# Performance work log

Hardware: AMD Instinct MI355X
Metric: run time of the kernel (lower is better)

## Reference

```python
import jax, jax.numpy as jnp
import numpy as np

D_MODEL = 1024
NUM_HEADS = 16
THETA = 10000.0
B, T = 2, 2048


def _rope(x, pos, theta_base):
    # x: (b, h, t, d_h); interleaved pairs (x0,x1),(x2,x3),... per the
    # rearrange '... (c d) -> ... c d' with d=2 in the original module.
    d = x.shape[-1]
    half = d // 2
    inv_freq = 1.0 / (theta_base ** (2.0 * jnp.arange(half, dtype=jnp.float32) / d))
    ang = pos.astype(jnp.float32)[:, None] * inv_freq[None, :]  # (t, half)
    sin = jnp.sin(ang)[None, None]  # (1,1,t,half)
    cos = jnp.cos(ang)[None, None]
    x1 = x[..., 0::2]
    x2 = x[..., 1::2]
    r1 = x1 * cos - x2 * sin
    r2 = x1 * sin + x2 * cos
    return jnp.stack([r1, r2], axis=-1).reshape(x.shape)


def setup_inputs() -> dict:
    key = jax.random.key(0)
    k0, k1, k2, k3, k4 = jax.random.split(key, 5)
    sigma = (2.0 / (D_MODEL + D_MODEL)) ** 0.5
    return {
        "in_features": jax.random.normal(k0, (B, T, D_MODEL), dtype=jnp.float32),
        "Wq": jax.random.normal(k1, (D_MODEL, D_MODEL), dtype=jnp.float32) * sigma,
        "Wk": jax.random.normal(k2, (D_MODEL, D_MODEL), dtype=jnp.float32) * sigma,
        "Wv": jax.random.normal(k3, (D_MODEL, D_MODEL), dtype=jnp.float32) * sigma,
        "Wo": jax.random.normal(k4, (D_MODEL, D_MODEL), dtype=jnp.float32) * sigma,
        "token_positions": jnp.arange(T, dtype=jnp.int32),
    }


def reference(in_features, Wq, Wk, Wv, Wo, token_positions):
    b, t, d_model = in_features.shape
    h = NUM_HEADS
    d_h = d_model // h
    # Fused-style QKV projections (x @ W.T, weights stored (in, out))
    q = in_features @ Wq.T
    k = in_features @ Wk.T
    v = in_features @ Wv.T
    # (b, t, h*d_h) -> (b, h, t, d_h)
    q = q.reshape(b, t, h, d_h).transpose(0, 2, 1, 3)
    k = k.reshape(b, t, h, d_h).transpose(0, 2, 1, 3)
    v = v.reshape(b, t, h, d_h).transpose(0, 2, 1, 3)
    q = _rope(q, token_positions, THETA)
    k = _rope(k, token_positions, THETA)
    scale = 1.0 / jnp.sqrt(jnp.asarray(d_h, dtype=q.dtype))
    scores = jnp.einsum('bhqd,bhkd->bhqk', q, k) * scale
    causal = jnp.tril(jnp.ones((t, t), dtype=bool))
    scores = jnp.where(causal[None, None], scores, -jnp.inf)
    attn = jax.nn.softmax(scores, axis=-1)
    out = jnp.einsum('bhqk,bhkd->bhqd', attn, v)
    out = out.transpose(0, 2, 1, 3).reshape(b, t, h * d_h)
    return out @ Wo.T
```

## Files before the change

### kernel.cpp

```cpp
#include <hip/hip_runtime.h>

#define D_MODEL 1024
#define NUM_HEADS 16
#define DH 64
#define B_SZ 2
#define T_SZ 2048
#define M_ROWS (B_SZ * T_SZ)

typedef __bf16 bf16;
typedef __bf16 bf16x4 __attribute__((ext_vector_type(4)));
typedef __bf16 bf16x8 __attribute__((ext_vector_type(8)));
typedef float f32x4 __attribute__((ext_vector_type(4)));

__device__ __forceinline__ void async_copy16(const bf16* g, bf16* l) {
  __builtin_amdgcn_global_load_lds(
      (const __attribute__((address_space(1))) void*)g,
      (__attribute__((address_space(3))) void*)l, 16, 0, 0);
}

#define NX (M_ROWS * D_MODEL / 4)
#define NW (D_MODEL * D_MODEL / 4)

__global__ __launch_bounds__(256) void cast_all(
    const float* __restrict__ X, const float* __restrict__ Wq,
    const float* __restrict__ Wk, const float* __restrict__ Wv,
    const float* __restrict__ Wo,
    bf16* __restrict__ Xb, bf16* __restrict__ Wqb, bf16* __restrict__ Wkb,
    bf16* __restrict__ Wvb, bf16* __restrict__ Wob) {
  int i = blockIdx.x * 256 + threadIdx.x;
  const float* s; bf16* d; int off;
  if (i < NX) {
    s = X; d = Xb; off = i;
  } else {
    int j = i - NX;
    int w = j >> 18;
    off = j & (NW - 1);
    if (w == 0)      { s = Wq; d = Wqb; }
    else if (w == 1) { s = Wk; d = Wkb; }
    else if (w == 2) { s = Wv; d = Wvb; }
    else             { s = Wo; d = Wob; }
  }
  float4 v = ((const float4*)s)[off];
  bf16x4 o;
  o[0] = (bf16)v.x; o[1] = (bf16)v.y; o[2] = (bf16)v.z; o[3] = (bf16)v.w;
  ((bf16x4*)d)[off] = o;
}

#define KLN 0.28782313662425f
#define BK 32
#define NKT (D_MODEL / BK)

__global__ __launch_bounds__(512, 4) void qkv_gemm(
    const bf16* __restrict__ Xb,
    const bf16* __restrict__ Wqb, const bf16* __restrict__ Wkb,
    const bf16* __restrict__ Wvb, const int* __restrict__ pos,
    bf16* __restrict__ Q, bf16* __restrict__ K, bf16* __restrict__ VT) {
  __shared__ bf16 LA[3][128 * BK];
  __shared__ bf16 LB[3][256 * BK];

  int tid = threadIdx.x;
  int wave = tid >> 6, lane = tid & 63;
  int wm = wave >> 2, wn = wave & 3;
  int l15 = lane & 15, quad = lane >> 4;

  int row0 = blockIdx.x * 128;
  int col0 = blockIdx.y * 256;
  int sel = col0 >> 10;
  int nb = col0 & 1023;
  const bf16* W = (sel == 0) ? Wqb : (sel == 1) ? Wkb : Wvb;

  int srow = tid >> 2;
  int scol = 8 * ((tid & 3) ^ ((tid >> 3) & 3));
  const bf16* Ag = Xb + (size_t)(row0 + srow) * D_MODEL + scol;
  const bf16* Bg = W + (size_t)(nb + srow) * D_MODEL + scol;
  int ldst = tid * 8;

  int swz = 8 * (quad ^ ((l15 >> 1) & 3));
  int aoff = (wm * 64 + l15) * BK + swz;
  int boff = (wn * 64 + l15) * BK + swz;

  f32x4 acc[4][4];
#pragma unroll
  for (int mi = 0; mi < 4; ++mi)
#pragma unroll
    for (int nj = 0; nj < 4; ++nj) acc[mi][nj] = (f32x4){0.f, 0.f, 0.f, 0.f};

#define STAGE(bq, pt)                                                        \
  do {                                                                       \
    int k0_ = (pt) * BK;                                                     \
    async_copy16(Ag + k0_, &LA[bq][ldst]);                                   \
    async_copy16(Bg + k0_, &LB[bq][ldst]);                                   \
    async_copy16(Bg + k0_ + (size_t)128 * D_MODEL, &LB[bq][ldst + 4096]);    \
  } while (0)

  STAGE(0, 0);
  STAGE(1, 1);
  asm volatile("s_waitcnt vmcnt(3)" ::: "memory");
  __builtin_amdgcn_s_barrier();
  __builtin_amdgcn_sched_barrier(0);

  int cur = 0;
  for (int kt = 0; kt < NKT; ++kt) {
    const bf16* La = LA[cur];
    const bf16* Lb = LB[cur];
    bf16x8 a[4], b[4];
#pragma unroll
    for (int mi = 0; mi < 4; ++mi)
      a[mi] = *(const bf16x8*)&La[aoff + mi * 16 * BK];
#pragma unroll
    for (int nj = 0; nj < 4; ++nj)
      b[nj] = *(const bf16x8*)&Lb[boff + nj * 16 * BK];

    if (kt + 2 < NKT) {
      int nbuf = cur + 2 >= 3 ? cur - 1 : cur + 2;
      STAGE(nbuf, kt + 2);
      asm volatile("s_waitcnt vmcnt(3) lgkmcnt(0)" ::: "memory");
    } else {
      asm volatile("s_waitcnt vmcnt(0) lgkmcnt(0)" ::: "memory");
    }
    __builtin_amdgcn_s_barrier();
    __builtin_amdgcn_sched_barrier(0);

    __builtin_amdgcn_s_setprio(1);
#pragma unroll
    for (int mi = 0; mi < 4; ++mi)
#pragma unroll
      for (int nj = 0; nj < 4; ++nj)
        acc[mi][nj] = __builtin_amdgcn_mfma_f32_16x16x32_bf16(
            a[mi], b[nj], acc[mi][nj], 0, 0, 0);
    __builtin_amdgcn_s_setprio(0);

    cur = cur == 2 ? 0 : cur + 1;
  }
#undef STAGE

  if (sel == 1) {
    bool even = (l15 & 1) == 0;
#pragma unroll
    for (int nj = 0; nj < 4; ++nj) {
      float fr = __expf(-(float)((nj * 16 + (l15 & 14)) >> 1) * KLN);
#pragma unroll
      for (int mi = 0; mi < 4; ++mi)
#pragma unroll
        for (int r = 0; r < 4; ++r) {
          float p = (float)pos[(row0 + wm * 64 + mi * 16 + quad * 4 + r) &
                               (T_SZ - 1)];
          float v = acc[mi][nj][r];
          float pn = __shfl_xor(v, 1);
          float s, c;
          __sincosf(p * fr, &s, &c);
          acc[mi][nj][r] = even ? (v * c - pn * s) : (pn * s + v * c);
        }
    }
  }

  if (sel == 2) {
    int b = row0 >> 11;
    int t0 = row0 & (T_SZ - 1);
#pragma unroll
    for (int mi = 0; mi < 4; ++mi) {
      int t = t0 + wm * 64 + mi * 16 + quad * 4;
#pragma unroll
      for (int nj = 0; nj < 4; ++nj) {
        int col = nb + wn * 64 + nj * 16 + l15;
        int h = col >> 6;
        int d = col & 63;
        bf16x4 ov;
#pragma unroll
        for (int r = 0; r < 4; ++r) ov[r] = (bf16)acc[mi][nj][r];
        *(bf16x4*)&VT[((size_t)(b * NUM_HEADS + h) * DH + d) * T_SZ + t] = ov;
      }
    }
  } else {
    bf16* Out = (sel == 0) ? Q : K;
#pragma unroll
    for (int mi = 0; mi < 4; ++mi) {
      int row = row0 + wm * 64 + mi * 16 + quad * 4;
#pragma unroll
      for (int nj = 0; nj < 4; ++nj) {
        int col = nb + wn * 64 + nj * 16 + l15;
#pragma unroll
        for (int r = 0; r < 4; ++r)
          Out[(size_t)(row + r) * D_MODEL + col] = (bf16)acc[mi][nj][r];
      }
    }
  }
}

#define PST 72
#define KST 72

__global__ __launch_bounds__(256) void attn_kernel(
    const bf16* __restrict__ Q, const bf16* __restrict__ K,
    const bf16* __restrict__ VT, const int* __restrict__ pos,
    bf16* __restrict__ AO) {
  __shared__ bf16 Kt[64 * KST];
  __shared__ bf16 Vt[64 * KST];
  __shared__ bf16 Pbuf[4][16 * PST];

  int bh = blockIdx.x;
  int y = blockIdx.y;
  int yq = y >> 3, yr = y & 7;
  int qi = 8 * yq + ((yq & 1) ? 7 - yr : yr);
  int bb = bh >> 4, h = bh & 15;
  int tid = threadIdx.x;
  int wave = tid >> 6, lane = tid & 63;
  int l15 = lane & 15, quad = lane >> 4;

  int q0 = qi * 64 + wave * 16;
  size_t grow = (size_t)bb * T_SZ + q0;

  const bf16* Qp = Q + (grow + l15) * D_MODEL + h * DH + quad * 8;
  bf16x8 bq0 = *(const bf16x8*)(Qp);
  bf16x8 bq1 = *(const bf16x8*)(Qp + 32);
  {
    float p = (float)pos[q0 + l15];
#pragma unroll
    for (int jj = 0; jj < 4; ++jj) {
      int i0 = quad * 4 + jj;
      float s, c;
      __sincosf(p * __expf(-(float)i0 * KLN), &s, &c);
      float x1 = (float)bq0[2 * jj], x2 = (float)bq0[2 * jj + 1];
      bq0[2 * jj]     = (bf16)(x1 * c - x2 * s);
      bq0[2 * jj + 1] = (bf16)(x1 * s + x2 * c);
      __sincosf(p * __expf(-(float)(i0 + 16) * KLN), &s, &c);
      float y1 = (float)bq1[2 * jj], y2 = (float)bq1[2 * jj + 1];
      bq1[2 * jj]     = (bf16)(y1 * c - y2 * s);
      bq1[2 * jj + 1] = (bf16)(y1 * s + y2 * c);
    }
  }

  f32x4 o[4];
#pragma unroll
  for (int nt = 0; nt < 4; ++nt) o[nt] = (f32x4){0.f, 0.f, 0.f, 0.f};
  float l_i = 0.f;

  int srow = tid >> 2;
  int sc = (tid & 3) * 16;
  const bf16* Kg = K + ((size_t)bb * T_SZ + srow) * D_MODEL + h * DH + sc;
  const bf16* Vg = VT + ((size_t)bh * DH + srow) * T_SZ + sc;
  bf16* Kl = &Kt[srow * KST + sc];
  bf16* Vl = &Vt[srow * KST + sc];

  bf16* Pw = Pbuf[wave];
  int nchunks = qi + 1;
  int rel = wave * 16 + l15;

  bf16x8 kr0 = *(const bf16x8*)(Kg);
  bf16x8 kr1 = *(const bf16x8*)(Kg + 8);
  bf16x8 vr0 = *(const bf16x8*)(Vg);
  bf16x8 vr1 = *(const bf16x8*)(Vg + 8);

  for (int t = 0; t < nchunks; ++t) {
    __syncthreads();
    *(bf16x8*)(Kl) = kr0;
    *(bf16x8*)(Kl + 8) = kr1;
    *(bf16x8*)(Vl) = vr0;
    *(bf16x8*)(Vl + 8) = vr1;
    if (t + 1 < nchunks) {
      const bf16* Kn = Kg + (size_t)(t + 1) * 64 * D_MODEL;
      const bf16* Vn = Vg + (t + 1) * 64;
      kr0 = *(const bf16x8*)(Kn);
      kr1 = *(const bf16x8*)(Kn + 8);
      vr0 = *(const bf16x8*)(Vn);
      vr1 = *(const bf16x8*)(Vn + 8);
    }
    __syncthreads();

    f32x4 st[4];
#pragma unroll
    for (int cs = 0; cs < 4; ++cs) {
      bf16x8 ak0 = *(const bf16x8*)&Kt[(cs * 16 + l15) * KST + quad * 8];
      bf16x8 ak1 = *(const bf16x8*)&Kt[(cs * 16 + l15) * KST + 32 + quad * 8];
      f32x4 s4 = (f32x4){0.f, 0.f, 0.f, 0.f};
      s4 = __builtin_amdgcn_mfma_f32_16x16x32_bf16(ak0, bq0, s4, 0, 0, 0);
      s4 = __builtin_amdgcn_mfma_f32_16x16x32_bf16(ak1, bq1, s4, 0, 0, 0);
      st[cs] = s4;
    }

    bool last = (t == nchunks - 1);
    float ps = 0.f;
#pragma unroll
    for (int cs = 0; cs < 4; ++cs)
#pragma unroll
      for (int r = 0; r < 4; ++r) {
        float p = __expf(st[cs][r] * 0.125f);
        if (last) {
          int cl = cs * 16 + quad * 4 + r;
          p = (cl > rel) ? 0.f : p;
        }
        st[cs][r] = p;
        ps += p;
      }
    l_i += ps;

#pragma unroll
    for (int cs = 0; cs < 4; ++cs) {
      bf16x4 pk;
#pragma unroll
      for (int r = 0; r < 4; ++r) pk[r] = (bf16)st[cs][r];
      *(bf16x4*)&Pw[l15 * PST + cs * 16 + quad * 4] = pk;
    }
    __asm__ __volatile__("" ::: "memory");
    bf16x8 bp0 = *(const bf16x8*)&Pw[l15 * PST + quad * 8];
    bf16x8 bp1 = *(const bf16x8*)&Pw[l15 * PST + 32 + quad * 8];
    __asm__ __volatile__("" ::: "memory");

#pragma unroll
    for (int nt = 0; nt < 4; ++nt) {
      bf16x8 av0 = *(const bf16x8*)&Vt[(nt * 16 + l15) * KST + quad * 8];
      bf16x8 av1 = *(const bf16x8*)&Vt[(nt * 16 + l15) * KST + 32 + quad * 8];
      o[nt] = __builtin_amdgcn_mfma_f32_16x16x32_bf16(av0, bp0, o[nt], 0, 0, 0);
      o[nt] = __builtin_amdgcn_mfma_f32_16x16x32_bf16(av1, bp1, o[nt], 0, 0, 0);
    }
  }

  l_i += __shfl_xor(l_i, 16);
  l_i += __shfl_xor(l_i, 32);
  float inv = 1.0f / l_i;
#pragma unroll
  for (int nt = 0; nt < 4; ++nt) {
    bf16x4 ov;
#pragma unroll
    for (int r = 0; r < 4; ++r) ov[r] = (bf16)(o[nt][r] * inv);
    *(bf16x4*)&AO[(grow + l15) * D_MODEL + h * DH + nt * 16 + quad * 4] = ov;
  }
}

__global__ __launch_bounds__(256) void out_gemm(
    const bf16* __restrict__ AO, const bf16* __restrict__ Wob,
    float* __restrict__ out) {
  __shared__ bf16 As[128 * 32];
  __shared__ bf16 Bs[64 * 32];

  int tid = threadIdx.x;
  int wave = tid >> 6, lane = tid & 63;
  int l15 = lane & 15, quad = lane >> 4;

  int row0 = blockIdx.x * 128;
  int nb = blockIdx.y * 64;

  int srow = tid >> 2;
  int schunk = tid & 3;
  const bf16* Ag = AO + (size_t)(row0 + srow) * D_MODEL + schunk * 8;
  const bf16* Bg = Wob + (size_t)(nb + srow) * D_MODEL + schunk * 8;
  bf16* Al0 = &As[srow * 32 + schunk * 8];
  bf16* Al1 = &As[(srow + 64) * 32 + schunk * 8];
  bf16* Bl = &Bs[srow * 32 + schunk * 8];

  f32x4 acc[2][4];
#pragma unroll
  for (int i = 0; i < 2; ++i)
#pragma unroll
    for (int j = 0; j < 4; ++j) acc[i][j] = (f32x4){0.f, 0.f, 0.f, 0.f};

  for (int k0 = 0; k0 < D_MODEL; k0 += 32) {
    async_copy16(Ag + k0, Al0);
    async_copy16(Ag + k0 + (size_t)64 * D_MODEL, Al1);
    async_copy16(Bg + k0, Bl);
    __syncthreads();

    bf16x8 af[2], bfr[4];
#pragma unroll
    for (int i = 0; i < 2; ++i)
      af[i] = *(const bf16x8*)&As[(wave * 32 + i * 16 + l15) * 32 + quad * 8];
#pragma unroll
    for (int j = 0; j < 4; ++j)
      bfr[j] = *(const bf16x8*)&Bs[(j * 16 + l15) * 32 + quad * 8];
#pragma unroll
    for (int i = 0; i < 2; ++i)
#pragma unroll
      for (int j = 0; j < 4; ++j)
        acc[i][j] = __builtin_amdgcn_mfma_f32_16x16x32_bf16(af[i], bfr[j],
                                                            acc[i][j], 0, 0, 0);
    __syncthreads();
  }

#pragma unroll
  for (int i = 0; i < 2; ++i) {
    int row = row0 + wave * 32 + i * 16 + quad * 4;
#pragma unroll
    for (int j = 0; j < 4; ++j) {
      int col = nb + j * 16 + l15;
#pragma unroll
      for (int r = 0; r < 4; ++r)
        out[(size_t)(row + r) * D_MODEL + col] = acc[i][j][r];
    }
  }
}

extern "C" void kernel_launch(void* const* d_in, const int* in_sizes, int n_in,
                              void* d_out, int out_size, void* d_ws, size_t ws_size,
                              hipStream_t stream) {
  const float* X  = (const float*)d_in[0];
  const float* Wq = (const float*)d_in[1];
  const float* Wk = (const float*)d_in[2];
  const float* Wv = (const float*)d_in[3];
  const float* Wo = (const float*)d_in[4];
  const int*  pos = (const int*)d_in[5];
  float* out = (float*)d_out;

  char* w = (char*)d_ws;
  bf16* Xb  = (bf16*)w;  w += (size_t)M_ROWS * D_MODEL * 2;
  bf16* Wqb = (bf16*)w;  w += (size_t)D_MODEL * D_MODEL * 2;
  bf16* Wkb = (bf16*)w;  w += (size_t)D_MODEL * D_MODEL * 2;
  bf16* Wvb = (bf16*)w;  w += (size_t)D_MODEL * D_MODEL * 2;
  bf16* Wob = (bf16*)w;  w += (size_t)D_MODEL * D_MODEL * 2;
  bf16* Qb  = (bf16*)w;  w += (size_t)M_ROWS * D_MODEL * 2;
  bf16* Kb  = (bf16*)w;  w += (size_t)M_ROWS * D_MODEL * 2;
  bf16* VT  = (bf16*)w;  w += (size_t)M_ROWS * D_MODEL * 2;
  bf16* AO  = (bf16*)w;  w += (size_t)M_ROWS * D_MODEL * 2;

  cast_all<<<(NX + 4 * NW) / 256, 256, 0, stream>>>(X, Wq, Wk, Wv, Wo,
                                                    Xb, Wqb, Wkb, Wvb, Wob);
  qkv_gemm<<<dim3(M_ROWS / 128, 3 * D_MODEL / 256), 512, 0, stream>>>(
      Xb, Wqb, Wkb, Wvb, pos, Qb, Kb, VT);
  attn_kernel<<<dim3(B_SZ * NUM_HEADS, T_SZ / 64), 256, 0, stream>>>(
      Qb, Kb, VT, pos, AO);
  out_gemm<<<dim3(M_ROWS / 128, D_MODEL / 64), 256, 0, stream>>>(AO, Wob, out);
}
```

Baseline: 174.9 us.

## Split attention keys across waves so P stays in registers, reduce partial outputs

Each wave now handles a 16-key slice of every 64-key chunk for all 64 queries, rather than 16 queries against all keys. The probabilities therefore come out in the register layout the 16x16x16 MFMA needs for the PV product, which removes the per-wave LDS round trip for P. The four waves' partial outputs and row sums are combined at the end through shared memory, at the cost of several extra barriers and a larger accumulator footprint. The query-block order is also changed to a simple largest-first schedule, and launch bounds now request 3 blocks per SM.

```diff
diff --git a/kernel.cpp b/kernel.cpp
--- a/kernel.cpp
+++ b/kernel.cpp
@@ -187,53 +187,56 @@
   }
 }
 
-#define PST 72
 #define KST 72
 
-__global__ __launch_bounds__(256) void attn_kernel(
+__global__ __launch_bounds__(256, 3) void attn_kernel(
     const bf16* __restrict__ Q, const bf16* __restrict__ K,
     const bf16* __restrict__ VT, const int* __restrict__ pos,
     bf16* __restrict__ AO) {
-  __shared__ bf16 Kt[64 * KST];
-  __shared__ bf16 Vt[64 * KST];
-  __shared__ bf16 Pbuf[4][16 * PST];
+  __shared__ bf16 KV[2 * 64 * KST];
+  __shared__ float lred[4][4][16];
+  bf16* Kt = KV;
+  bf16* Vt = KV + 64 * KST;
 
   int bh = blockIdx.x;
-  int y = blockIdx.y;
-  int yq = y >> 3, yr = y & 7;
-  int qi = 8 * yq + ((yq & 1) ? 7 - yr : yr);
+  int qi = 31 - (int)blockIdx.y;
   int bb = bh >> 4, h = bh & 15;
   int tid = threadIdx.x;
   int wave = tid >> 6, lane = tid & 63;
   int l15 = lane & 15, quad = lane >> 4;
-
-  int q0 = qi * 64 + wave * 16;
+  int w16 = wave * 16;
+
+  int q0 = qi * 64;
   size_t grow = (size_t)bb * T_SZ + q0;
 
-  const bf16* Qp = Q + (grow + l15) * D_MODEL + h * DH + quad * 8;
-  bf16x8 bq0 = *(const bf16x8*)(Qp);
-  bf16x8 bq1 = *(const bf16x8*)(Qp + 32);
-  {
-    float p = (float)pos[q0 + l15];
+  bf16x8 bq[4][2];
+#pragma unroll
+  for (int qt = 0; qt < 4; ++qt) {
+    const bf16* Qp = Q + (grow + qt * 16 + l15) * D_MODEL + h * DH + quad * 8;
+    bq[qt][0] = *(const bf16x8*)(Qp);
+    bq[qt][1] = *(const bf16x8*)(Qp + 32);
+    float p = (float)pos[q0 + qt * 16 + l15];
 #pragma unroll
     for (int jj = 0; jj < 4; ++jj) {
       int i0 = quad * 4 + jj;
       float s, c;
       __sincosf(p * __expf(-(float)i0 * KLN), &s, &c);
-      float x1 = (float)bq0[2 * jj], x2 = (float)bq0[2 * jj + 1];
-      bq0[2 * jj]     = (bf16)(x1 * c - x2 * s);
-      bq0[2 * jj + 1] = (bf16)(x1 * s + x2 * c);
+      float x1 = (float)bq[qt][0][2 * jj], x2 = (float)bq[qt][0][2 * jj + 1];
+      bq[qt][0][2 * jj]     = (bf16)(x1 * c - x2 * s);
+      bq[qt][0][2 * jj + 1] = (bf16)(x1 * s + x2 * c);
       __sincosf(p * __expf(-(float)(i0 + 16) * KLN), &s, &c);
-      float y1 = (float)bq1[2 * jj], y2 = (float)bq1[2 * jj + 1];
-      bq1[2 * jj]     = (bf16)(y1 * c - y2 * s);
-      bq1[2 * jj + 1] = (bf16)(y1 * s + y2 * c);
-    }
-  }
-
-  f32x4 o[4];
-#pragma unroll
-  for (int nt = 0; nt < 4; ++nt) o[nt] = (f32x4){0.f, 0.f, 0.f, 0.f};
-  float l_i = 0.f;
+      float y1 = (float)bq[qt][1][2 * jj], y2 = (float)bq[qt][1][2 * jj + 1];
+      bq[qt][1][2 * jj]     = (bf16)(y1 * c - y2 * s);
+      bq[qt][1][2 * jj + 1] = (bf16)(y1 * s + y2 * c);
+    }
+  }
+
+  f32x4 o[4][4];
+#pragma unroll
+  for (int dt = 0; dt < 4; ++dt)
+#pragma unroll
+    for (int qt = 0; qt < 4; ++qt) o[dt][qt] = (f32x4){0.f, 0.f, 0.f, 0.f};
+  float l_acc[4] = {0.f, 0.f, 0.f, 0.f};
 
   int srow = tid >> 2;
   int sc = (tid & 3) * 16;
@@ -242,9 +245,7 @@
   bf16* Kl = &Kt[srow * KST + sc];
   bf16* Vl = &Vt[srow * KST + sc];
 
-  bf16* Pw = Pbuf[wave];
   int nchunks = qi + 1;
-  int rel = wave * 16 + l15;
 
   bf16x8 kr0 = *(const bf16x8*)(Kg);
   bf16x8 kr1 = *(const bf16x8*)(Kg + 8);
@@ -267,64 +268,97 @@
     }
     __syncthreads();
 
+    bf16x8 ak0 = *(const bf16x8*)&Kt[(w16 + l15) * KST + quad * 8];
+    bf16x8 ak1 = *(const bf16x8*)&Kt[(w16 + l15) * KST + 32 + quad * 8];
     f32x4 st[4];
 #pragma unroll
-    for (int cs = 0; cs < 4; ++cs) {
-      bf16x8 ak0 = *(const bf16x8*)&Kt[(cs * 16 + l15) * KST + quad * 8];
-      bf16x8 ak1 = *(const bf16x8*)&Kt[(cs * 16 + l15) * KST + 32 + quad * 8];
+    for (int qt = 0; qt < 4; ++qt) {
       f32x4 s4 = (f32x4){0.f, 0.f, 0.f, 0.f};
-      s4 = __builtin_amdgcn_mfma_f32_16x16x32_bf16(ak0, bq0, s4, 0, 0, 0);
-      s4 = __builtin_amdgcn_mfma_f32_16x16x32_bf16(ak1, bq1, s4, 0, 0, 0);
-      st[cs] = s4;
+      s4 = __builtin_amdgcn_mfma_f32_16x16x32_bf16(ak0, bq[qt][0], s4, 0, 0, 0);
+      s4 = __builtin_amdgcn_mfma_f32_16x16x32_bf16(ak1, bq[qt][1], s4, 0, 0, 0);
+      st[qt] = s4;
     }
 
     bool last = (t == nchunks - 1);
-    float ps = 0.f;
-#pragma unroll
-    for (int cs = 0; cs < 4; ++cs)
+    bf16x4 pb[4];
+#pragma unroll
+    for (int qt = 0; qt < 4; ++qt) {
+      float ps = 0.f;
+#pragma unroll
+      for (int j = 0; j < 4; ++j) {
+        float p = __expf(st[qt][j] * 0.125f);
+        if (last) {
+          int cl = w16 + quad * 4 + j;
+          p = (cl > qt * 16 + l15) ? 0.f : p;
+        }
+        pb[qt][j] = (bf16)p;
+        ps += p;
+      }
+      l_acc[qt] += ps;
+    }
+
+#pragma unroll
+    for (int dt = 0; dt < 4; ++dt) {
+      bf16x4 vb = *(const bf16x4*)&Vt[(dt * 16 + l15) * KST + w16 + quad * 4];
+#pragma unroll
+      for (int qt = 0; qt < 4; ++qt)
+        asm("v_mfma_f32_16x16x16_bf16 %0, %1, %2, %0"
+            : "+v"(o[dt][qt])
+            : "v"(pb[qt]), "v"(vb));
+    }
+  }
+
+#pragma unroll
+  for (int qt = 0; qt < 4; ++qt) {
+    l_acc[qt] += __shfl_xor(l_acc[qt], 16);
+    l_acc[qt] += __shfl_xor(l_acc[qt], 32);
+  }
+  if (lane < 16) {
+#pragma unroll
+    for (int qt = 0; qt < 4; ++qt) lred[wave][qt][lane] = l_acc[qt];
+  }
+
+  __syncthreads();
+  float* red = (float*)KV;
+
+#pragma unroll
+  for (int s = 1; s <= 3; ++s) {
+#pragma unroll
+    for (int qt = 0; qt < 4; ++qt)
+      if (((qt - s) & 3) == wave) {
+#pragma unroll
+        for (int dt = 0; dt < 4; ++dt)
+          *(f32x4*)&red[qt * 1024 + dt * 256 + lane * 4] = o[dt][qt];
+      }
+    __syncthreads();
+#pragma unroll
+    for (int qt = 0; qt < 4; ++qt)
+      if (qt == wave) {
+#pragma unroll
+        for (int dt = 0; dt < 4; ++dt)
+          o[dt][qt] += *(const f32x4*)&red[qt * 1024 + dt * 256 + lane * 4];
+      }
+    __syncthreads();
+  }
+
+#pragma unroll
+  for (int qt = 0; qt < 4; ++qt)
+    if (qt == wave) {
+      float inv[4];
 #pragma unroll
       for (int r = 0; r < 4; ++r) {
-        float p = __expf(st[cs][r] * 0.125f);
-        if (last) {
-          int cl = cs * 16 + quad * 4 + r;
-          p = (cl > rel) ? 0.f : p;
-        }
-        st[cs][r] = p;
-        ps += p;
-      }
-    l_i += ps;
-
-#pragma unroll
-    for (int cs = 0; cs < 4; ++cs) {
-      bf16x4 pk;
-#pragma unroll
-      for (int r = 0; r < 4; ++r) pk[r] = (bf16)st[cs][r];
-      *(bf16x4*)&Pw[l15 * PST + cs * 16 + quad * 4] = pk;
-    }
-    __asm__ __volatile__("" ::: "memory");
-    bf16x8 bp0 = *(const bf16x8*)&Pw[l15 * PST + quad * 8];
-    bf16x8 bp1 = *(const bf16x8*)&Pw[l15 * PST + 32 + quad * 8];
-    __asm__ __volatile__("" ::: "memory");
-
-#pragma unroll
-    for (int nt = 0; nt < 4; ++nt) {
-      bf16x8 av0 = *(const bf16x8*)&Vt[(nt * 16 + l15) * KST + quad * 8];
-      bf16x8 av1 = *(const bf16x8*)&Vt[(nt * 16 + l15) * KST + 32 + quad * 8];
-      o[nt] = __builtin_amdgcn_mfma_f32_16x16x32_bf16(av0, bp0, o[nt], 0, 0, 0);
-      o[nt] = __builtin_amdgcn_mfma_f32_16x16x32_bf16(av1, bp1, o[nt], 0, 0, 0);
-    }
-  }
-
-  l_i += __shfl_xor(l_i, 16);
-  l_i += __shfl_xor(l_i, 32);
-  float inv = 1.0f / l_i;
-#pragma unroll
-  for (int nt = 0; nt < 4; ++nt) {
-    bf16x4 ov;
-#pragma unroll
-    for (int r = 0; r < 4; ++r) ov[r] = (bf16)(o[nt][r] * inv);
-    *(bf16x4*)&AO[(grow + l15) * D_MODEL + h * DH + nt * 16 + quad * 4] = ov;
-  }
+        int qq = quad * 4 + r;
+        float ls = lred[0][qt][qq] + lred[1][qt][qq] + lred[2][qt][qq] +
+                   lred[3][qt][qq];
+        inv[r] = 1.0f / ls;
+      }
+#pragma unroll
+      for (int dt = 0; dt < 4; ++dt)
+#pragma unroll
+        for (int r = 0; r < 4; ++r)
+          AO[(grow + qt * 16 + quad * 4 + r) * D_MODEL + h * DH + dt * 16 +
+             l15] = (bf16)(o[dt][qt][r] * inv[r]);
+    }
 }
 
 __global__ __launch_bounds__(256) void out_gemm(
```

New measurement: 173.0 us. Within noise of the previous version (-1.1%).
